# Kernel optimization log

Hardware: AMD Instinct MI355X
Metric: run time of the kernel (lower is better)

## Reference

```python
import jax, jax.numpy as jnp
import numpy as np

D_MODEL = 1024
LN_EPS = 1e-5


def setup_inputs() -> dict:
    key = jax.random.key(0)
    ks = jax.random.split(key, 12)
    d = D_MODEL
    std_qkv = np.sqrt(2.0 / (d + d / 16)).astype(np.float32)
    std_fc = np.sqrt(2.0 / (d + d)).astype(np.float32)  # xavier_normal for square matrix
    inp = {
        "x": jax.random.normal(ks[0], (2, 2048, d), dtype=jnp.float32),
        "Wq": jax.random.normal(ks[1], (d, d), dtype=jnp.float32) * std_qkv,
        "bq": jnp.zeros((d,), dtype=jnp.float32),
        "Wk": jax.random.normal(ks[2], (d, d), dtype=jnp.float32) * std_qkv,
        "bk": jnp.zeros((d,), dtype=jnp.float32),
        "Wv": jax.random.normal(ks[3], (d, d), dtype=jnp.float32) * std_qkv,
        "bv": jnp.zeros((d,), dtype=jnp.float32),
        "Wfc": jax.random.normal(ks[4], (d, d), dtype=jnp.float32) * std_fc,
        "bfc": jnp.zeros((d,), dtype=jnp.float32),
        "gamma": jnp.ones((d,), dtype=jnp.float32),
        "beta": jnp.zeros((d,), dtype=jnp.float32),
        "n_heads": 16,
    }
    return inp


def reference(x, Wq, bq, Wk, bk, Wv, bv, Wfc, bfc, gamma, beta, n_heads):
    b, l, d = x.shape
    dk = d // n_heads

    def proj2(t, W, bias):
        # Faithful to original: projection applied TWICE (w_qs(w_qs(input)) etc.)
        t = t @ W.T + bias
        return t @ W.T + bias

    def split_heads(t):
        # b l (h dk) -> h b l dk
        return t.reshape(b, l, n_heads, dk).transpose(2, 0, 1, 3)

    q = split_heads(proj2(x, Wq, bq))
    k = split_heads(proj2(x, Wk, bk))
    v = split_heads(proj2(x, Wv, bv))

    scores = jnp.einsum("hblk,hbtk->hblt", q, k) / np.sqrt(dk).astype(np.float32)
    attn = jax.nn.softmax(scores, axis=3)
    out = jnp.einsum("hblt,hbtv->hblv", attn, v)
    out = out.transpose(1, 2, 0, 3).reshape(b, l, d)  # h b l v -> b l (h v)
    out = out @ Wfc.T + bfc  # dropout = identity in eval
    out = out + x

    mu = jnp.mean(out, axis=-1, keepdims=True)
    var = jnp.mean(jnp.square(out - mu), axis=-1, keepdims=True)
    out = (out - mu) * jax.lax.rsqrt(var + LN_EPS) * gamma + beta
    return (out, attn)
```

## Files before the change

kernel.cpp:

```cpp
#include <hip/hip_runtime.h>
#include <hip/hip_bf16.h>

typedef unsigned short u16;
typedef float  f32x4  __attribute__((ext_vector_type(4)));
typedef short  bf16x8 __attribute__((ext_vector_type(8)));
typedef u16    u16x4  __attribute__((ext_vector_type(4)));
typedef u16    u16x8  __attribute__((ext_vector_type(8)));

__device__ __forceinline__ u16 f2bf(float f) {
    union { __hip_bfloat16 b; u16 u; } c;
    c.b = __float2bfloat16(f);
    return c.u;
}
__device__ __forceinline__ float bf2f(u16 u) {
    union { unsigned i; float f; } c;
    c.i = ((unsigned)u) << 16;
    return c.f;
}

__device__ __forceinline__ void gl2lds16(const u16* g, u16* l) {
    __builtin_amdgcn_global_load_lds(
        (const __attribute__((address_space(1))) void*)g,
        (__attribute__((address_space(3))) void*)l,
        16, 0, 0);
}

__global__ __launch_bounds__(256) void convk(const float* __restrict__ src,
                                             u16* __restrict__ dst, int n4) {
    int i = blockIdx.x * 256 + threadIdx.x;
    if (i < n4) {
        float4 v = ((const float4*)src)[i];
        u16x4 o = { f2bf(v.x), f2bf(v.y), f2bf(v.z), f2bf(v.w) };
        ((u16x4*)dst)[i] = o;
    }
}

__global__ __launch_bounds__(256) void convW(const float* __restrict__ Wq,
                                             const float* __restrict__ Wk,
                                             const float* __restrict__ Wv,
                                             const float* __restrict__ Wfc,
                                             u16* __restrict__ Wallb,
                                             u16* __restrict__ Wfcb) {
    const int z = blockIdx.y;
    const float* src = z == 0 ? Wq : z == 1 ? Wk : z == 2 ? Wv : Wfc;
    u16* dst = z < 3 ? Wallb + (size_t)z * 1048576 : Wfcb;
    int i = blockIdx.x * 256 + threadIdx.x;
    float4 v = ((const float4*)src)[i];
    u16x4 o = { f2bf(v.x), f2bf(v.y), f2bf(v.z), f2bf(v.w) };
    ((u16x4*)dst)[i] = o;
}

__global__ __launch_bounds__(256) void transkB(const float* __restrict__ Wq,
                                               const float* __restrict__ Wk,
                                               const float* __restrict__ Wv,
                                               u16* __restrict__ Wallt) {
    const int z = blockIdx.z;
    const float* src = z == 0 ? Wq : z == 1 ? Wk : Wv;
    u16* dst = Wallt + (size_t)z * 1048576;
    __shared__ u16 t[64][72];
    const int tr = blockIdx.x * 64, tc = blockIdx.y * 64;
    const int r4 = threadIdx.x >> 4;
    const int c4 = (threadIdx.x & 15) * 4;
#pragma unroll
    for (int rr = 0; rr < 4; ++rr) {
        int r = rr * 16 + r4;
        float4 v = *(const float4*)&src[(size_t)(tr + r) * 1024 + tc + c4];
        t[r][c4] = f2bf(v.x); t[r][c4 + 1] = f2bf(v.y);
        t[r][c4 + 2] = f2bf(v.z); t[r][c4 + 3] = f2bf(v.w);
    }
    __syncthreads();
#pragma unroll
    for (int rr = 0; rr < 4; ++rr) {
        int oc = rr * 16 + r4;
        u16x4 o = { t[c4][oc], t[c4 + 1][oc], t[c4 + 2][oc], t[c4 + 3][oc] };
        *(u16x4*)&dst[(size_t)(tc + oc) * 1024 + tr + c4] = o;
    }
}

__global__ __launch_bounds__(256) void transV(const u16* __restrict__ QKV,
                                              u16* __restrict__ VT) {
    const int kt = blockIdx.x, bb = blockIdx.y, h = blockIdx.z;
    __shared__ u16 t[64][72];
    const int tid = threadIdx.x;
    {
        const int key = tid >> 3, d8 = (tid & 7) * 8;
        const u16* src = QKV + 2048 +
            ((size_t)(bb * 2048 + kt * 64 + key)) * 3072 + h * 64 + d8;
        *(u16x8*)&t[key][d8]      = *(const u16x8*)src;
        *(u16x8*)&t[key + 32][d8] = *(const u16x8*)(src + (size_t)32 * 3072);
    }
    __syncthreads();
    {
        const int dk = tid >> 3, k8 = (tid & 7) * 8;
        u16* dst = VT + ((size_t)((bb * 16 + h) * 64 + dk)) * 2048 + kt * 64 + k8;
        u16x8 o0, o1;
#pragma unroll
        for (int j = 0; j < 8; ++j) { o0[j] = t[k8 + j][dk]; o1[j] = t[k8 + j][dk + 32]; }
        *(u16x8*)dst = o0;
        *(u16x8*)(dst + (size_t)32 * 2048) = o1;
    }
}

__global__ __launch_bounds__(256) void bias2(const float* __restrict__ Wq, const float* __restrict__ bq,
                                             const float* __restrict__ Wk, const float* __restrict__ bk,
                                             const float* __restrict__ Wv, const float* __restrict__ bv,
                                             float* __restrict__ out) {
    const int z = blockIdx.y;
    const float* W = z == 0 ? Wq : z == 1 ? Wk : Wv;
    const float* b = z == 0 ? bq : z == 1 ? bk : bv;
    const int row  = blockIdx.x * 4 + (threadIdx.x >> 6);
    const int lane = threadIdx.x & 63;
    float4 w  = ((const float4*)(W + (size_t)row * 1024))[lane];
    float4 bb = ((const float4*)b)[lane];
    float s = w.x * bb.x + w.y * bb.y + w.z * bb.z + w.w * bb.w;
#pragma unroll
    for (int d = 1; d < 64; d <<= 1) s += __shfl_xor(s, d);
    if (lane == 0) out[z * 1024 + row] = s + b[row];
}

template<int OUTF32>
__global__ __launch_bounds__(256) void gemm_bt(const u16* __restrict__ A,
                                               const u16* __restrict__ B,
                                               const float* __restrict__ bias,
                                               void* __restrict__ Cout,
                                               int M, int N, int K,
                                               size_t zA, size_t zB, size_t zC,
                                               const float* __restrict__ xres) {
    __shared__ __align__(16) u16 As[128 * 32];
    __shared__ __align__(16) u16 Bs[128 * 32];

    const int tid  = threadIdx.x;
    const int lane = tid & 63;
    const int w    = tid >> 6;
    const int lr   = lane & 15;
    const int lg   = lane >> 4;
    const int wr   = (w >> 1) * 64;
    const int wc   = (w & 1) * 64;
    const int bm   = blockIdx.x * 128;
    const int bn   = blockIdx.y * 128;
    const int z    = blockIdx.z;
    A += (size_t)z * zA;
    B += (size_t)z * zB;
    char* Cz = (char*)Cout + (size_t)z * zC * (OUTF32 ? 4 : 2);

    const int srow = w * 32 + (lane >> 2);
    const int scol = (lane & 3) * 8;
    u16* la = &As[(w * 32) * 32];
    u16* lb = &Bs[(w * 32) * 32];

    f32x4 acc[4][4] = {};

    for (int k0 = 0; k0 < K; k0 += 32) {
        const u16* Ag = A + (size_t)(bm + srow) * K + k0 + scol;
        const u16* Bg = B + (size_t)(bn + srow) * K + k0 + scol;
        gl2lds16(Ag, la);
        gl2lds16(Ag + (size_t)16 * K, la + 16 * 32);
        gl2lds16(Bg, lb);
        gl2lds16(Bg + (size_t)16 * K, lb + 16 * 32);
        __syncthreads();

        bf16x8 af[4], bfr[4];
#pragma unroll
        for (int i = 0; i < 4; ++i)
            af[i] = *(const bf16x8*)&As[(wr + i * 16 + lr) * 32 + lg * 8];
#pragma unroll
        for (int j = 0; j < 4; ++j)
            bfr[j] = *(const bf16x8*)&Bs[(wc + j * 16 + lr) * 32 + lg * 8];
#pragma unroll
        for (int i = 0; i < 4; ++i)
#pragma unroll
            for (int j = 0; j < 4; ++j)
                acc[i][j] = __builtin_amdgcn_mfma_f32_16x16x32_bf16(
                    af[i], bfr[j], acc[i][j], 0, 0, 0);
        __syncthreads();
    }

#pragma unroll
    for (int i = 0; i < 4; ++i) {
        const int grow = bm + wr + i * 16 + lg * 4;
#pragma unroll
        for (int j = 0; j < 4; ++j) {
            const int gcol = bn + wc + j * 16 + lr;
            const float bv = bias ? bias[gcol] : 0.f;
#pragma unroll
            for (int r = 0; r < 4; ++r) {
                float v = acc[i][j][r] + bv;
                if (OUTF32) {
                    if (xres) v += xres[(size_t)(grow + r) * N + gcol];
                    ((float*)Cz)[(size_t)(grow + r) * N + gcol] = v;
                } else {
                    ((u16*)Cz)[(size_t)(grow + r) * N + gcol] = f2bf(v);
                }
            }
        }
    }
}

__global__ __launch_bounds__(256, 4) void attn5(const u16* __restrict__ QKV,
                                                const u16* __restrict__ VT,
                                                float* __restrict__ P,
                                                u16* __restrict__ O) {
    const int hw  = blockIdx.x;
    const int L   = (hw & 7) * 128 + (hw >> 3);
    const int qb  = L & 31;
    const int bbh = L >> 5;
    const int bb  = bbh >> 4;
    const int h   = bbh & 15;
    const int tid = threadIdx.x, lane = tid & 63, w = tid >> 6;
    const int lr = lane & 15, lg = lane >> 4;

    __shared__ __align__(16) u16 smem[20480];

    const int qrow0 = qb * 64 + w * 16;
    const size_t qoff = ((size_t)bb * 2048 + qrow0 + lr) * 3072 + h * 64 + lg * 8;
    const bf16x8 qf0 = *(const bf16x8*)&QKV[qoff];
    const bf16x8 qf1 = *(const bf16x8*)&QKV[qoff + 32];

    const int srow  = lane >> 3;
    const int sslot = (lane & 7) ^ srow;
    const u16* kg0 = QKV + 1024 + ((size_t)bb * 2048 + w * 16 + srow) * 3072 + h * 64 + sslot * 8;
    const u16* vg0 = VT + ((size_t)((bb * 16 + h) * 64) + w * 16 + srow) * 2048 + sslot * 8;

    const int swz   = (lr & 7) << 3;
    const int offk0 = (lg * 8) ^ swz;
    const int offk1 = (32 + lg * 8) ^ swz;
    const int rowB  = lr * 64;
    const float SC  = 0.18033688011112042f;

    auto stageKto = [&](int kt, int ldsOff) {
        const u16* s = kg0 + (size_t)kt * 64 * 3072;
        gl2lds16(s,                    smem + ldsOff + (w * 16) * 64);
        gl2lds16(s + (size_t)8 * 3072, smem + ldsOff + (w * 16 + 8) * 64);
    };
    auto stageVto = [&](int kt, int ldsOff) {
        const u16* s = vg0 + kt * 64;
        gl2lds16(s,                    smem + ldsOff + (w * 16) * 64);
        gl2lds16(s + (size_t)8 * 2048, smem + ldsOff + (w * 16 + 8) * 64);
    };

    float lsum[4] = {0.f, 0.f, 0.f, 0.f};
    stageKto(0, 0);
    stageKto(1, 4096);
    for (int kt = 0; kt < 32; ++kt) {
        if (kt < 31) asm volatile("s_waitcnt vmcnt(2)" ::: "memory");
        else         asm volatile("s_waitcnt vmcnt(0)" ::: "memory");
        __builtin_amdgcn_s_barrier();
        const u16* Kb = smem + (kt % 3) * 4096;
        __builtin_amdgcn_s_setprio(1);
#pragma unroll
        for (int jb = 0; jb < 4; ++jb) {
            bf16x8 kf0 = *(const bf16x8*)&Kb[jb * 1024 + rowB + offk0];
            bf16x8 kf1 = *(const bf16x8*)&Kb[jb * 1024 + rowB + offk1];
            f32x4 acc = {0.f, 0.f, 0.f, 0.f};
            acc = __builtin_amdgcn_mfma_f32_16x16x32_bf16(qf0, kf0, acc, 0, 0, 0);
            acc = __builtin_amdgcn_mfma_f32_16x16x32_bf16(qf1, kf1, acc, 0, 0, 0);
#pragma unroll
            for (int r = 0; r < 4; ++r)
                lsum[r] += __builtin_amdgcn_exp2f(acc[r] * SC);
        }
        __builtin_amdgcn_s_setprio(0);
        if (kt < 30) stageKto(kt + 2, ((kt + 2) % 3) * 4096);
    }
#pragma unroll
    for (int r = 0; r < 4; ++r) {
#pragma unroll
        for (int d = 1; d < 16; d <<= 1) lsum[r] += __shfl_xor(lsum[r], d);
    }
    float rl[4];
#pragma unroll
    for (int r = 0; r < 4; ++r) rl[r] = 1.f / lsum[r];

    __syncthreads();

    f32x4 oacc[4] = {};
    const size_t prowb = (size_t)(h * 2 + bb) * 2048 + qrow0;
    const int wrow = lane >> 4;
    const int wcol = (lane & 15) * 4;
    u16* Psw = smem + 16384 + w * 1024;

    stageKto(0, 0); stageVto(0, 8192);
    for (int kt = 0; kt < 32; ++kt) {
        const int cur = kt & 1;
        if (kt == 0) {
            stageKto(1, 4096); stageVto(1, 12288);
            asm volatile("s_waitcnt vmcnt(4)" ::: "memory");
        } else if (kt < 31) {
            stageKto(kt + 1, (cur ^ 1) * 4096);
            stageVto(kt + 1, 8192 + (cur ^ 1) * 4096);
            asm volatile("s_waitcnt vmcnt(8)" ::: "memory");
        } else {
            asm volatile("s_waitcnt vmcnt(4)" ::: "memory");
        }
        __builtin_amdgcn_s_barrier();

        const u16* Kb = smem + cur * 4096;
        const u16* Vb = smem + 8192 + cur * 4096;

        __builtin_amdgcn_s_setprio(1);
#pragma unroll
        for (int jb = 0; jb < 4; ++jb) {
            bf16x8 kf0 = *(const bf16x8*)&Kb[jb * 1024 + rowB + offk0];
            bf16x8 kf1 = *(const bf16x8*)&Kb[jb * 1024 + rowB + offk1];
            f32x4 acc = {0.f, 0.f, 0.f, 0.f};
            acc = __builtin_amdgcn_mfma_f32_16x16x32_bf16(qf0, kf0, acc, 0, 0, 0);
            acc = __builtin_amdgcn_mfma_f32_16x16x32_bf16(qf1, kf1, acc, 0, 0, 0);
#pragma unroll
            for (int r = 0; r < 4; ++r) {
                float p = __builtin_amdgcn_exp2f(acc[r] * SC) * rl[r];
                const int row = lg * 4 + r;
                Psw[row * 64 + ((jb * 16 + lr) ^ ((row & 7) << 3))] = f2bf(p);
            }
        }
        __builtin_amdgcn_s_setprio(0);
#pragma unroll
        for (int rr = 0; rr < 4; ++rr) {
            const int row = rr * 4 + wrow;
            const int s = wcol >> 3, e = wcol & 7;
            u16x4 pb = *(const u16x4*)&Psw[row * 64 + ((s ^ (row & 7)) * 8) + e];
            f32x4 pv = { bf2f(pb[0]), bf2f(pb[1]), bf2f(pb[2]), bf2f(pb[3]) };
            __builtin_nontemporal_store(pv,
                (f32x4*)&P[(prowb + row) * 2048 + kt * 64 + wcol]);
        }
        __builtin_amdgcn_s_setprio(1);
#pragma unroll
        for (int kk = 0; kk < 2; ++kk) {
            const int offk = kk ? offk1 : offk0;
            bf16x8 pa = *(const bf16x8*)&Psw[rowB + offk];
#pragma unroll
            for (int dkb = 0; dkb < 4; ++dkb) {
                bf16x8 vb = *(const bf16x8*)&Vb[dkb * 1024 + rowB + offk];
                oacc[dkb] = __builtin_amdgcn_mfma_f32_16x16x32_bf16(pa, vb, oacc[dkb], 0, 0, 0);
            }
        }
        __builtin_amdgcn_s_setprio(0);
        __builtin_amdgcn_s_barrier();
    }

#pragma unroll
    for (int dkb = 0; dkb < 4; ++dkb)
#pragma unroll
        for (int r = 0; r < 4; ++r)
            O[((size_t)bb * 2048 + qrow0 + lg * 4 + r) * 1024 + h * 64 + dkb * 16 + lr] =
                f2bf(oacc[dkb][r]);
}

__global__ __launch_bounds__(256) void ln_only(float* __restrict__ Y,
                                               const float* __restrict__ gamma,
                                               const float* __restrict__ beta) {
    const int row = blockIdx.x, tid = threadIdx.x;
    const int lane = tid & 63, w = tid >> 6;
    float4 y = ((const float4*)(Y + (size_t)row * 1024))[tid];
    float t0 = y.x, t1 = y.y, t2 = y.z, t3 = y.w;
    float s  = t0 + t1 + t2 + t3;
    float ss = t0 * t0 + t1 * t1 + t2 * t2 + t3 * t3;
#pragma unroll
    for (int d = 1; d < 64; d <<= 1) { s += __shfl_xor(s, d); ss += __shfl_xor(ss, d); }
    __shared__ float as_[4], aq_[4];
    if (lane == 0) { as_[w] = s; aq_[w] = ss; }
    __syncthreads();
    s  = as_[0] + as_[1] + as_[2] + as_[3];
    ss = aq_[0] + aq_[1] + aq_[2] + aq_[3];
    const float mu  = s * (1.f / 1024.f);
    const float var = ss * (1.f / 1024.f) - mu * mu;
    const float rs  = rsqrtf(var + 1e-5f);
    float4 g  = ((const float4*)gamma)[tid];
    float4 be = ((const float4*)beta)[tid];
    float4 o;
    o.x = (t0 - mu) * rs * g.x + be.x;
    o.y = (t1 - mu) * rs * g.y + be.y;
    o.z = (t2 - mu) * rs * g.z + be.z;
    o.w = (t3 - mu) * rs * g.w + be.w;
    ((float4*)(Y + (size_t)row * 1024))[tid] = o;
}

extern "C" void kernel_launch(void* const* d_in, const int* in_sizes, int n_in,
                              void* d_out, int out_size, void* d_ws, size_t ws_size,
                              hipStream_t stream) {
    const float* x     = (const float*)d_in[0];
    const float* Wq    = (const float*)d_in[1];
    const float* bq    = (const float*)d_in[2];
    const float* Wk    = (const float*)d_in[3];
    const float* bk    = (const float*)d_in[4];
    const float* Wv    = (const float*)d_in[5];
    const float* bv    = (const float*)d_in[6];
    const float* Wfc   = (const float*)d_in[7];
    const float* bfc   = (const float*)d_in[8];
    const float* gamma = (const float*)d_in[9];
    const float* beta  = (const float*)d_in[10];

    float* out  = (float*)d_out;
    float* attn = out + (size_t)4194304;

    u16* VT = (u16*)d_out;

    char* ws = (char*)d_ws;
    u16* QKV  = (u16*)(ws);
    u16* Ob   = (u16*)(ws + (size_t)24 * 1048576);
    u16* Wfcb = (u16*)(ws + (size_t)32 * 1048576);

    char* sc = (char*)attn;
    u16*   Xb    = (u16*)sc;
    u16*   Wallb = (u16*)(sc + (size_t)8  * 1048576);
    u16*   Wallt = (u16*)(sc + (size_t)14 * 1048576);
    u16*   Wall2 = (u16*)(sc + (size_t)20 * 1048576);
    float* ball2 = (float*)(sc + (size_t)26 * 1048576);

    const size_t WSZ = 1048576;

    convk<<<4096, 256, 0, stream>>>(x, Xb, 1048576);
    convW<<<dim3(1024, 4), 256, 0, stream>>>(Wq, Wk, Wv, Wfc, Wallb, Wfcb);
    transkB<<<dim3(16, 16, 3), 256, 0, stream>>>(Wq, Wk, Wv, Wallt);
    bias2<<<dim3(256, 3), 256, 0, stream>>>(Wq, bq, Wk, bk, Wv, bv, ball2);

    const dim3 blk(256);
    gemm_bt<0><<<dim3(8, 8, 3), blk, 0, stream>>>(Wallb, Wallt, nullptr, Wall2,
                                                  1024, 1024, 1024, WSZ, WSZ, WSZ, nullptr);
    gemm_bt<0><<<dim3(32, 24), blk, 0, stream>>>(Xb, Wall2, ball2, QKV,
                                                 4096, 3072, 1024, 0, 0, 0, nullptr);

    transV<<<dim3(32, 2, 16), 256, 0, stream>>>(QKV, VT);
    attn5<<<1024, 256, 0, stream>>>(QKV, VT, attn, Ob);

    gemm_bt<1><<<dim3(32, 8), blk, 0, stream>>>(Ob, Wfcb, bfc, out,
                                                4096, 1024, 1024, 0, 0, 0, x);
    ln_only<<<4096, 256, 0, stream>>>(out, gamma, beta);
}
```

Measured before the change: 280.8 us.

## Merge prep kernels and split softmax row-sum into separate kernel

The four preprocessing kernels (x and weight bf16 conversion, weight transpose, bias folding) become one launch that dispatches on block index. The attention kernel's first pass, which computes softmax denominators, moves to its own kernel. That kernel handles 32 query rows per wave so each staged K tile is reused across two query groups, and it writes reciprocal sums to a scratch region of the output. The attention kernel then reads these and only computes P and O. This cuts launch overhead and halves K traffic for the row-sum pass, at the cost of an extra launch and a global round trip for the row sums.

```diff
diff --git a/kernel.cpp b/kernel.cpp
--- a/kernel.cpp
+++ b/kernel.cpp
@@ -25,55 +25,70 @@
         16, 0, 0);
 }
 
-__global__ __launch_bounds__(256) void convk(const float* __restrict__ src,
-                                             u16* __restrict__ dst, int n4) {
-    int i = blockIdx.x * 256 + threadIdx.x;
-    if (i < n4) {
-        float4 v = ((const float4*)src)[i];
+__global__ __launch_bounds__(256) void prep(const float* __restrict__ x,
+                                            const float* __restrict__ Wq,
+                                            const float* __restrict__ bq,
+                                            const float* __restrict__ Wk,
+                                            const float* __restrict__ bk,
+                                            const float* __restrict__ Wv,
+                                            const float* __restrict__ bv,
+                                            const float* __restrict__ Wfc,
+                                            u16* __restrict__ Xb,
+                                            u16* __restrict__ Wallb,
+                                            u16* __restrict__ Wfcb,
+                                            u16* __restrict__ Wallt,
+                                            float* __restrict__ ball2) {
+    const int b = blockIdx.x, tid = threadIdx.x;
+    __shared__ u16 t[64][72];
+    if (b < 4096) {
+        int i = b * 256 + tid;
+        float4 v = ((const float4*)x)[i];
         u16x4 o = { f2bf(v.x), f2bf(v.y), f2bf(v.z), f2bf(v.w) };
-        ((u16x4*)dst)[i] = o;
-    }
-}
-
-__global__ __launch_bounds__(256) void convW(const float* __restrict__ Wq,
-                                             const float* __restrict__ Wk,
-                                             const float* __restrict__ Wv,
-                                             const float* __restrict__ Wfc,
-                                             u16* __restrict__ Wallb,
-                                             u16* __restrict__ Wfcb) {
-    const int z = blockIdx.y;
-    const float* src = z == 0 ? Wq : z == 1 ? Wk : z == 2 ? Wv : Wfc;
-    u16* dst = z < 3 ? Wallb + (size_t)z * 1048576 : Wfcb;
-    int i = blockIdx.x * 256 + threadIdx.x;
-    float4 v = ((const float4*)src)[i];
-    u16x4 o = { f2bf(v.x), f2bf(v.y), f2bf(v.z), f2bf(v.w) };
-    ((u16x4*)dst)[i] = o;
-}
-
-__global__ __launch_bounds__(256) void transkB(const float* __restrict__ Wq,
-                                               const float* __restrict__ Wk,
-                                               const float* __restrict__ Wv,
-                                               u16* __restrict__ Wallt) {
-    const int z = blockIdx.z;
-    const float* src = z == 0 ? Wq : z == 1 ? Wk : Wv;
-    u16* dst = Wallt + (size_t)z * 1048576;
-    __shared__ u16 t[64][72];
-    const int tr = blockIdx.x * 64, tc = blockIdx.y * 64;
-    const int r4 = threadIdx.x >> 4;
-    const int c4 = (threadIdx.x & 15) * 4;
-#pragma unroll
-    for (int rr = 0; rr < 4; ++rr) {
-        int r = rr * 16 + r4;
-        float4 v = *(const float4*)&src[(size_t)(tr + r) * 1024 + tc + c4];
-        t[r][c4] = f2bf(v.x); t[r][c4 + 1] = f2bf(v.y);
-        t[r][c4 + 2] = f2bf(v.z); t[r][c4 + 3] = f2bf(v.w);
-    }
-    __syncthreads();
-#pragma unroll
-    for (int rr = 0; rr < 4; ++rr) {
-        int oc = rr * 16 + r4;
-        u16x4 o = { t[c4][oc], t[c4 + 1][oc], t[c4 + 2][oc], t[c4 + 3][oc] };
-        *(u16x4*)&dst[(size_t)(tc + oc) * 1024 + tr + c4] = o;
+        ((u16x4*)Xb)[i] = o;
+    } else if (b < 8192) {
+        int i = b - 4096;
+        int z = i >> 10, blk = i & 1023;
+        const float* src = z == 0 ? Wq : z == 1 ? Wk : z == 2 ? Wv : Wfc;
+        u16* dst = z < 3 ? Wallb + (size_t)z * 1048576 : Wfcb;
+        int j = blk * 256 + tid;
+        float4 v = ((const float4*)src)[j];
+        u16x4 o = { f2bf(v.x), f2bf(v.y), f2bf(v.z), f2bf(v.w) };
+        ((u16x4*)dst)[j] = o;
+    } else if (b < 8960) {
+        int i = b - 8192;
+        int z = i >> 8, rem = i & 255;
+        const float* src = z == 0 ? Wq : z == 1 ? Wk : Wv;
+        u16* dst = Wallt + (size_t)z * 1048576;
+        const int tr = (rem >> 4) * 64, tc = (rem & 15) * 64;
+        const int r4 = tid >> 4;
+        const int c4 = (tid & 15) * 4;
+#pragma unroll
+        for (int rr = 0; rr < 4; ++rr) {
+            int r = rr * 16 + r4;
+            float4 v = *(const float4*)&src[(size_t)(tr + r) * 1024 + tc + c4];
+            t[r][c4] = f2bf(v.x); t[r][c4 + 1] = f2bf(v.y);
+            t[r][c4 + 2] = f2bf(v.z); t[r][c4 + 3] = f2bf(v.w);
+        }
+        __syncthreads();
+#pragma unroll
+        for (int rr = 0; rr < 4; ++rr) {
+            int oc = rr * 16 + r4;
+            u16x4 o = { t[c4][oc], t[c4 + 1][oc], t[c4 + 2][oc], t[c4 + 3][oc] };
+            *(u16x4*)&dst[(size_t)(tc + oc) * 1024 + tr + c4] = o;
+        }
+    } else {
+        int i = b - 8960;
+        int z = i >> 8, bx = i & 255;
+        const float* W = z == 0 ? Wq : z == 1 ? Wk : Wv;
+        const float* bias = z == 0 ? bq : z == 1 ? bk : bv;
+        const int row  = bx * 4 + (tid >> 6);
+        const int lane = tid & 63;
+        float4 w  = ((const float4*)(W + (size_t)row * 1024))[lane];
+        float4 bb = ((const float4*)bias)[lane];
+        float s = w.x * bb.x + w.y * bb.y + w.z * bb.z + w.w * bb.w;
+#pragma unroll
+        for (int d = 1; d < 64; d <<= 1) s += __shfl_xor(s, d);
+        if (lane == 0) ball2[z * 1024 + row] = s + bias[row];
     }
 }
 
@@ -99,23 +114,6 @@
         *(u16x8*)dst = o0;
         *(u16x8*)(dst + (size_t)32 * 2048) = o1;
     }
-}
-
-__global__ __launch_bounds__(256) void bias2(const float* __restrict__ Wq, const float* __restrict__ bq,
-                                             const float* __restrict__ Wk, const float* __restrict__ bk,
-                                             const float* __restrict__ Wv, const float* __restrict__ bv,
-                                             float* __restrict__ out) {
-    const int z = blockIdx.y;
-    const float* W = z == 0 ? Wq : z == 1 ? Wk : Wv;
-    const float* b = z == 0 ? bq : z == 1 ? bk : bv;
-    const int row  = blockIdx.x * 4 + (threadIdx.x >> 6);
-    const int lane = threadIdx.x & 63;
-    float4 w  = ((const float4*)(W + (size_t)row * 1024))[lane];
-    float4 bb = ((const float4*)b)[lane];
-    float s = w.x * bb.x + w.y * bb.y + w.z * bb.z + w.w * bb.w;
-#pragma unroll
-    for (int d = 1; d < 64; d <<= 1) s += __shfl_xor(s, d);
-    if (lane == 0) out[z * 1024 + row] = s + b[row];
 }
 
 template<int OUTF32>
@@ -196,10 +194,94 @@
     }
 }
 
-__global__ __launch_bounds__(256, 4) void attn5(const u16* __restrict__ QKV,
-                                                const u16* __restrict__ VT,
-                                                float* __restrict__ P,
-                                                u16* __restrict__ O) {
+__global__ __launch_bounds__(256, 4) void lsumK(const u16* __restrict__ QKV,
+                                                float* __restrict__ rl_g) {
+    const int hw  = blockIdx.x;
+    const int L   = (hw & 7) * 64 + (hw >> 3);
+    const int qb  = L & 15;
+    const int bbh = L >> 4;
+    const int bb  = bbh >> 4;
+    const int h   = bbh & 15;
+    const int tid = threadIdx.x, lane = tid & 63, w = tid >> 6;
+    const int lr = lane & 15, lg = lane >> 4;
+
+    __shared__ __align__(16) u16 smem[12288];
+
+    const int qrow0 = qb * 128 + w * 32;
+    bf16x8 qf[2][2];
+#pragma unroll
+    for (int qg = 0; qg < 2; ++qg) {
+        const size_t qoff =
+            ((size_t)bb * 2048 + qrow0 + qg * 16 + lr) * 3072 + h * 64 + lg * 8;
+        qf[qg][0] = *(const bf16x8*)&QKV[qoff];
+        qf[qg][1] = *(const bf16x8*)&QKV[qoff + 32];
+    }
+
+    const int srow  = lane >> 3;
+    const int sslot = (lane & 7) ^ srow;
+    const u16* kg0 = QKV + 1024 + ((size_t)bb * 2048 + w * 16 + srow) * 3072 + h * 64 + sslot * 8;
+
+    const int swz   = (lr & 7) << 3;
+    const int offk0 = (lg * 8) ^ swz;
+    const int offk1 = (32 + lg * 8) ^ swz;
+    const int rowB  = lr * 64;
+    const float SC  = 0.18033688011112042f;
+
+    auto stageKto = [&](int kt, int ldsOff) {
+        const u16* s = kg0 + (size_t)kt * 64 * 3072;
+        gl2lds16(s,                    smem + ldsOff + (w * 16) * 64);
+        gl2lds16(s + (size_t)8 * 3072, smem + ldsOff + (w * 16 + 8) * 64);
+    };
+
+    float lsum[2][4] = {};
+    stageKto(0, 0);
+    stageKto(1, 4096);
+    for (int kt = 0; kt < 32; ++kt) {
+        if (kt < 31) asm volatile("s_waitcnt vmcnt(2)" ::: "memory");
+        else         asm volatile("s_waitcnt vmcnt(0)" ::: "memory");
+        __builtin_amdgcn_s_barrier();
+        const u16* Kb = smem + (kt % 3) * 4096;
+        __builtin_amdgcn_s_setprio(1);
+#pragma unroll
+        for (int jb = 0; jb < 4; ++jb) {
+            bf16x8 kf0 = *(const bf16x8*)&Kb[jb * 1024 + rowB + offk0];
+            bf16x8 kf1 = *(const bf16x8*)&Kb[jb * 1024 + rowB + offk1];
+#pragma unroll
+            for (int qg = 0; qg < 2; ++qg) {
+                f32x4 acc = {0.f, 0.f, 0.f, 0.f};
+                acc = __builtin_amdgcn_mfma_f32_16x16x32_bf16(qf[qg][0], kf0, acc, 0, 0, 0);
+                acc = __builtin_amdgcn_mfma_f32_16x16x32_bf16(qf[qg][1], kf1, acc, 0, 0, 0);
+#pragma unroll
+                for (int r = 0; r < 4; ++r)
+                    lsum[qg][r] += __builtin_amdgcn_exp2f(acc[r] * SC);
+            }
+        }
+        __builtin_amdgcn_s_setprio(0);
+        if (kt < 30) stageKto(kt + 2, ((kt + 2) % 3) * 4096);
+    }
+#pragma unroll
+    for (int qg = 0; qg < 2; ++qg)
+#pragma unroll
+        for (int r = 0; r < 4; ++r) {
+#pragma unroll
+            for (int d = 1; d < 16; d <<= 1)
+                lsum[qg][r] += __shfl_xor(lsum[qg][r], d);
+        }
+    if (lr == 0) {
+        const size_t base = (size_t)(h * 2 + bb) * 2048 + qrow0;
+#pragma unroll
+        for (int qg = 0; qg < 2; ++qg)
+#pragma unroll
+            for (int r = 0; r < 4; ++r)
+                rl_g[base + qg * 16 + lg * 4 + r] = 1.f / lsum[qg][r];
+    }
+}
+
+__global__ __launch_bounds__(256, 4) void attnPO(const u16* __restrict__ QKV,
+                                                 const u16* __restrict__ VT,
+                                                 const float* __restrict__ rl_g,
+                                                 float* __restrict__ P,
+                                                 u16* __restrict__ O) {
     const int hw  = blockIdx.x;
     const int L   = (hw & 7) * 128 + (hw >> 3);
     const int qb  = L & 31;
@@ -215,6 +297,11 @@
     const size_t qoff = ((size_t)bb * 2048 + qrow0 + lr) * 3072 + h * 64 + lg * 8;
     const bf16x8 qf0 = *(const bf16x8*)&QKV[qoff];
     const bf16x8 qf1 = *(const bf16x8*)&QKV[qoff + 32];
+
+    const size_t prowb = (size_t)(h * 2 + bb) * 2048 + qrow0;
+    float rl[4];
+#pragma unroll
+    for (int r = 0; r < 4; ++r) rl[r] = rl_g[prowb + lg * 4 + r];
 
     const int srow  = lane >> 3;
     const int sslot = (lane & 7) ^ srow;
@@ -238,42 +325,7 @@
         gl2lds16(s + (size_t)8 * 2048, smem + ldsOff + (w * 16 + 8) * 64);
     };
 
-    float lsum[4] = {0.f, 0.f, 0.f, 0.f};
-    stageKto(0, 0);
-    stageKto(1, 4096);
-    for (int kt = 0; kt < 32; ++kt) {
-        if (kt < 31) asm volatile("s_waitcnt vmcnt(2)" ::: "memory");
-        else         asm volatile("s_waitcnt vmcnt(0)" ::: "memory");
-        __builtin_amdgcn_s_barrier();
-        const u16* Kb = smem + (kt % 3) * 4096;
-        __builtin_amdgcn_s_setprio(1);
-#pragma unroll
-        for (int jb = 0; jb < 4; ++jb) {
-            bf16x8 kf0 = *(const bf16x8*)&Kb[jb * 1024 + rowB + offk0];
-            bf16x8 kf1 = *(const bf16x8*)&Kb[jb * 1024 + rowB + offk1];
-            f32x4 acc = {0.f, 0.f, 0.f, 0.f};
-            acc = __builtin_amdgcn_mfma_f32_16x16x32_bf16(qf0, kf0, acc, 0, 0, 0);
-            acc = __builtin_amdgcn_mfma_f32_16x16x32_bf16(qf1, kf1, acc, 0, 0, 0);
-#pragma unroll
-            for (int r = 0; r < 4; ++r)
-                lsum[r] += __builtin_amdgcn_exp2f(acc[r] * SC);
-        }
-        __builtin_amdgcn_s_setprio(0);
-        if (kt < 30) stageKto(kt + 2, ((kt + 2) % 3) * 4096);
-    }
-#pragma unroll
-    for (int r = 0; r < 4; ++r) {
-#pragma unroll
-        for (int d = 1; d < 16; d <<= 1) lsum[r] += __shfl_xor(lsum[r], d);
-    }
-    float rl[4];
-#pragma unroll
-    for (int r = 0; r < 4; ++r) rl[r] = 1.f / lsum[r];
-
-    __syncthreads();
-
     f32x4 oacc[4] = {};
-    const size_t prowb = (size_t)(h * 2 + bb) * 2048 + qrow0;
     const int wrow = lane >> 4;
     const int wcol = (lane & 15) * 4;
     u16* Psw = smem + 16384 + w * 1024;
@@ -391,7 +443,8 @@
     float* out  = (float*)d_out;
     float* attn = out + (size_t)4194304;
 
-    u16* VT = (u16*)d_out;
+    u16*   VT   = (u16*)d_out;
+    float* rl_g = (float*)((char*)d_out + (size_t)9 * 1048576);
 
     char* ws = (char*)d_ws;
     u16* QKV  = (u16*)(ws);
@@ -407,10 +460,8 @@
 
     const size_t WSZ = 1048576;
 
-    convk<<<4096, 256, 0, stream>>>(x, Xb, 1048576);
-    convW<<<dim3(1024, 4), 256, 0, stream>>>(Wq, Wk, Wv, Wfc, Wallb, Wfcb);
-    transkB<<<dim3(16, 16, 3), 256, 0, stream>>>(Wq, Wk, Wv, Wallt);
-    bias2<<<dim3(256, 3), 256, 0, stream>>>(Wq, bq, Wk, bk, Wv, bv, ball2);
+    prep<<<9728, 256, 0, stream>>>(x, Wq, bq, Wk, bk, Wv, bv, Wfc,
+                                   Xb, Wallb, Wfcb, Wallt, ball2);
 
     const dim3 blk(256);
     gemm_bt<0><<<dim3(8, 8, 3), blk, 0, stream>>>(Wallb, Wallt, nullptr, Wall2,
@@ -418,8 +469,9 @@
     gemm_bt<0><<<dim3(32, 24), blk, 0, stream>>>(Xb, Wall2, ball2, QKV,
                                                  4096, 3072, 1024, 0, 0, 0, nullptr);
 
+    lsumK<<<512, 256, 0, stream>>>(QKV, rl_g);
     transV<<<dim3(32, 2, 16), 256, 0, stream>>>(QKV, VT);
-    attn5<<<1024, 256, 0, stream>>>(QKV, VT, attn, Ob);
+    attnPO<<<1024, 256, 0, stream>>>(QKV, VT, rl_g, attn, Ob);
 
     gemm_bt<1><<<dim3(32, 8), blk, 0, stream>>>(Ob, Wfcb, bfc, out,
                                                 4096, 1024, 1024, 0, 0, 0, x);
```

Result: no change. 281.3 us (+0.2%).
